# Kernel optimization log

Hardware: AMD Instinct MI355X
Metric: run time of the kernel (lower is better)

The kernel has to match this reference:

```python
import jax, jax.numpy as jnp
import numpy as np

EPS = 1e-9
N, E = 100000, 1000000
IN_F, OUT_F, HEADS = 128, 64, 2


def normalize_points(x):
    # UHG projective normalize: unit-norm spatial part, keep last (homogeneous) coord
    n = jnp.linalg.norm(x[..., :-1], axis=-1, keepdims=True)
    return jnp.concatenate([x[..., :-1] / jnp.maximum(n, EPS), x[..., -1:]], axis=-1)


def uhg_inner(a, b):
    # hyperbolic inner product: spatial dot minus time-time product
    return jnp.sum(a[..., :-1] * b[..., :-1], axis=-1) - a[..., -1] * b[..., -1]


def compute_cross_ratio(p1, p2, p3, p4):
    num = uhg_inner(p1, p3) * uhg_inner(p2, p4)
    den = uhg_inner(p1, p4) * uhg_inner(p2, p3)
    return num / jnp.where(jnp.abs(den) < EPS, EPS, den)


def restore_cross_ratio(x, cr_target):
    cr_cur = compute_cross_ratio(x[0], x[1], x[2], x[3])
    scale = jnp.abs(cr_target / jnp.where(jnp.abs(cr_cur) < EPS, EPS, cr_cur)) ** 0.25
    return x * scale


def setup_inputs() -> dict:
    key = jax.random.key(0)
    ks = jax.random.split(key, 10)
    s_in = 1.0 / np.sqrt(IN_F)
    s_hid = 1.0 / np.sqrt(OUT_F * HEADS)
    H = OUT_F * HEADS
    return {
        "x": jax.random.normal(ks[0], (N, IN_F), dtype=jnp.float32),
        "edge_index": jax.random.randint(ks[1], (2, E), 0, N, dtype=jnp.int64),
        "Wq": jax.random.uniform(ks[2], (H, IN_F), jnp.float32, -s_in, s_in),
        "bq": jnp.zeros((H,), jnp.float32),
        "Wk": jax.random.uniform(ks[3], (H, IN_F), jnp.float32, -s_in, s_in),
        "bk": jnp.zeros((H,), jnp.float32),
        "Wv": jax.random.uniform(ks[4], (H, IN_F), jnp.float32, -s_in, s_in),
        "bv": jnp.zeros((H,), jnp.float32),
        "Wo": jax.random.uniform(ks[5], (OUT_F, H), jnp.float32, -s_hid, s_hid),
        "bo": jnp.zeros((OUT_F,), jnp.float32),
    }


def reference(x, edge_index, Wq, bq, Wk, bk, Wv, bv, Wo, bo):
    n = x.shape[0]
    cr_initial = compute_cross_ratio(x[0], x[1], x[2], x[3])
    x_proj = normalize_points(x)
    q = (x_proj @ Wq.T + bq).reshape(n, HEADS, OUT_F)
    k = (x_proj @ Wk.T + bk).reshape(n, HEADS, OUT_F)
    v = (x_proj @ Wv.T + bv).reshape(n, HEADS, OUT_F)
    row, col = edge_index[0], edge_index[1]
    qe = normalize_points(q[row])  # [E, H, D]
    ke = normalize_points(k[col])
    scores = uhg_inner(qe, ke) / np.sqrt(IN_F)  # [E, H]
    alpha = jax.nn.softmax(scores, axis=0)  # global softmax over edges (as in source)
    msgs = v[col] * alpha[..., None]  # [E, H, D]
    out = jax.ops.segment_sum(msgs, row, num_segments=n)  # [N, H, D]
    out = out.reshape(n, HEADS * OUT_F)
    out = out @ Wo.T + bo
    out = restore_cross_ratio(out, cr_initial)
    return out
```

## Files before the change

### kernel.cpp

```cpp
#include <hip/hip_runtime.h>
#include <math.h>

#define EPSF 1e-9f
#define INV_SQRT128 0.08838834764831845f

typedef _Float16 half8 __attribute__((ext_vector_type(8)));
typedef float f32x4 __attribute__((ext_vector_type(4)));

__device__ __forceinline__ void gl_lds16(const void* g, void* l) {
    __builtin_amdgcn_global_load_lds((const __attribute__((address_space(1))) void*)g,
                                     (__attribute__((address_space(3))) void*)l, 16, 0, 0);
}

__global__ void k_wpack(const float* __restrict__ Wq, const float* __restrict__ Wk,
                        const float* __restrict__ Wv, half8* __restrict__ whi,
                        half8* __restrict__ wlo, float* __restrict__ w127) {
    int t = blockIdx.x * 256 + threadIdx.x;
    if (t >= 6144) return;
    int col = t & 127, g = (t >> 7) & 3, ks = (t >> 9) & 3, kind = t >> 11;
    const float* W = (kind == 0) ? Wq : (kind == 1) ? Wk : Wv;
    const float4* W4 = (const float4*)W;
    float4 a = W4[col * 32 + ks * 8 + g * 2];
    float4 b = W4[col * 32 + ks * 8 + g * 2 + 1];
    float xv[8] = {a.x, a.y, a.z, a.w, b.x, b.y, b.z, b.w};
    half8 h, lo;
#pragma unroll
    for (int j = 0; j < 8; j++) {
        _Float16 hh = (_Float16)xv[j];
        h[j] = hh;
        lo[j] = (_Float16)((xv[j] - (float)hh) * 4096.0f);
    }
    whi[t] = h;
    wlo[t] = lo;
    if (ks == 3 && g == 3) w127[kind * 128 + col] = xv[7];
}

__global__ void k_wpack2(const float* __restrict__ Wo, half8* __restrict__ wohi,
                         half8* __restrict__ wolo) {
    int t = blockIdx.x * 256 + threadIdx.x;
    if (t >= 1024) return;
    int col = t & 63, g = (t >> 6) & 3, ks = t >> 8;
    const float4* W4 = (const float4*)Wo;
    float4 a = W4[col * 32 + ks * 8 + g * 2];
    float4 b = W4[col * 32 + ks * 8 + g * 2 + 1];
    float xv[8] = {a.x, a.y, a.z, a.w, b.x, b.y, b.z, b.w};
    half8 h, lo;
#pragma unroll
    for (int j = 0; j < 8; j++) {
        _Float16 hh = (_Float16)xv[j];
        h[j] = hh;
        lo[j] = (_Float16)((xv[j] - (float)hh) * 4096.0f);
    }
    wohi[t] = h;
    wolo[t] = lo;
}

__global__ void __launch_bounds__(256, 2)
k_qkvm(const float* __restrict__ x,
       const half8* __restrict__ whi, const half8* __restrict__ wlo,
       const float* __restrict__ w127,
       const float* __restrict__ bq, const float* __restrict__ bk,
       const float* __restrict__ bv,
       float* __restrict__ qn, float* __restrict__ kvout,
       const int* __restrict__ ei, int* __restrict__ bcnt,
       int N, int E, int chunk) {
    int b = (int)blockIdx.x;
    __shared__ half8 bsh[4096];
    if (b < 512 && (b & 1)) {
        int* h = (int*)bsh;
        int t = threadIdx.x;
        int hid = b >> 1;
        h[t] = 0;
        __syncthreads();
        int s = hid * chunk, e1 = min(s + chunk, E);
        for (int e = s + t; e < e1; e += 256) atomicAdd(&h[ei[e] >> 9], 1);
        __syncthreads();
        bcnt[hid * 256 + t] = h[t];
        return;
    }
    int gb = (b < 512) ? (b >> 1) : (b - 256);

    int tid = threadIdx.x;
    int wv = tid >> 6;
    int l = tid & 63;
    int r = l & 15;
    int g = l >> 4;
    int rowbase = gb * 128 + wv * 32;
    const float4* x4 = (const float4*)x;

    {
        const half8* sH = whi + wv * 512;
        const half8* sL = wlo + wv * 512;
#pragma unroll
        for (int i = 0; i < 8; i++) {
            gl_lds16(sH + i * 64 + l, bsh + wv * 512 + i * 64);
            gl_lds16(sL + i * 64 + l, bsh + 2048 + wv * 512 + i * 64);
        }
    }

    half8 hiA[2][4], loA[2][4];
    float rnj[2][4], tcj[2][4];
#pragma unroll
    for (int t = 0; t < 2; t++) {
        int row = min(rowbase + t * 16 + r, N - 1);
        float ssum = 0.f, tl = 0.f;
#pragma unroll
        for (int ks = 0; ks < 4; ks++) {
            float4 a = x4[(size_t)row * 32 + ks * 8 + g * 2];
            float4 bb = x4[(size_t)row * 32 + ks * 8 + g * 2 + 1];
            float xv[8] = {a.x, a.y, a.z, a.w, bb.x, bb.y, bb.z, bb.w};
#pragma unroll
            for (int j = 0; j < 8; j++) {
                _Float16 hh = (_Float16)xv[j];
                hiA[t][ks][j] = hh;
                loA[t][ks][j] = (_Float16)((xv[j] - (float)hh) * 4096.0f);
                ssum += xv[j] * xv[j];
            }
            if (ks == 3 && g == 3) { tl = xv[7]; ssum -= xv[7] * xv[7]; }
        }
        ssum += __shfl_xor(ssum, 16);
        ssum += __shfl_xor(ssum, 32);
        float rn = 1.f / fmaxf(sqrtf(ssum), EPSF);
        float tla = __shfl(tl, 48 + r);
        float tc = tla * (1.f - rn);
#pragma unroll
        for (int j = 0; j < 4; j++) {
            rnj[t][j] = __shfl(rn, g * 4 + j);
            tcj[t][j] = __shfl(tc, g * 4 + j);
        }
    }

    asm volatile("s_waitcnt vmcnt(0)" ::: "memory");
    __syncthreads();

    const float* const bks[3] = {bq, bk, bv};
    bool lane15 = (r == 15);
    const f32x4 zz = {0.f, 0.f, 0.f, 0.f};
    int dsbase = g * 128 + r;

    for (int kind = 0; kind < 3; kind++) {
        float wcA[2][4], bbA[2][4];
#pragma unroll
        for (int h = 0; h < 2; h++)
#pragma unroll
            for (int ct = 0; ct < 4; ct++) {
                int col = (h * 4 + ct) * 16 + r;
                wcA[h][ct] = w127[kind * 128 + col];
                bbA[h][ct] = bks[kind][col];
            }

#pragma unroll
        for (int h = 0; h < 2; h++) {
            f32x4 aM[2][4], aX[2][4];
#pragma unroll
            for (int t = 0; t < 2; t++)
#pragma unroll
                for (int ct = 0; ct < 4; ct++) { aM[t][ct] = zz; aX[t][ct] = zz; }

#pragma unroll
            for (int ks = 0; ks < 4; ks++) {
                half8 hB[4], lB[4];
#pragma unroll
                for (int ct = 0; ct < 4; ct++) {
                    int bi = dsbase + ks * 512 + (h * 4 + ct) * 16;
                    hB[ct] = bsh[bi];
                    lB[ct] = bsh[2048 + bi];
                }
#pragma unroll
                for (int ct = 0; ct < 4; ct++) {
                    aM[0][ct] = __builtin_amdgcn_mfma_f32_16x16x32_f16(hiA[0][ks], hB[ct], aM[0][ct], 0, 0, 0);
                    aM[1][ct] = __builtin_amdgcn_mfma_f32_16x16x32_f16(hiA[1][ks], hB[ct], aM[1][ct], 0, 0, 0);
                    aX[0][ct] = __builtin_amdgcn_mfma_f32_16x16x32_f16(hiA[0][ks], lB[ct], aX[0][ct], 0, 0, 0);
                    aX[0][ct] = __builtin_amdgcn_mfma_f32_16x16x32_f16(loA[0][ks], hB[ct], aX[0][ct], 0, 0, 0);
                    aX[1][ct] = __builtin_amdgcn_mfma_f32_16x16x32_f16(hiA[1][ks], lB[ct], aX[1][ct], 0, 0, 0);
                    aX[1][ct] = __builtin_amdgcn_mfma_f32_16x16x32_f16(loA[1][ks], hB[ct], aX[1][ct], 0, 0, 0);
                }
            }

#pragma unroll
            for (int t = 0; t < 2; t++) {
                float cv[4][4];
#pragma unroll
                for (int ct = 0; ct < 4; ct++)
#pragma unroll
                    for (int j = 0; j < 4; j++) {
                        float acc = aM[t][ct][j] + aX[t][ct][j] * (1.0f / 4096.0f);
                        cv[ct][j] = fmaf(rnj[t][j], acc, fmaf(tcj[t][j], wcA[h][ct], bbA[h][ct]));
                    }
                if (kind < 2) {
#pragma unroll
                    for (int j = 0; j < 4; j++) {
                        float ss = 0.f;
#pragma unroll
                        for (int ct = 0; ct < 4; ct++) {
                            float c = cv[ct][j];
                            ss += (ct == 3 && lane15) ? 0.f : c * c;
                        }
                        ss += __shfl_xor(ss, 1);
                        ss += __shfl_xor(ss, 2);
                        ss += __shfl_xor(ss, 4);
                        ss += __shfl_xor(ss, 8);
                        float rh = 1.f / fmaxf(sqrtf(ss), EPSF);
#pragma unroll
                        for (int ct = 0; ct < 4; ct++) {
                            bool ist = (ct == 3) && lane15;
                            if (!ist) cv[ct][j] *= rh;
                            if (kind == 0) {
                                if (ist) cv[ct][j] = -cv[ct][j];
                                cv[ct][j] *= INV_SQRT128;
                            }
                        }
                    }
                }
#pragma unroll
                for (int j = 0; j < 4; j++) {
                    int row = rowbase + t * 16 + g * 4 + j;
                    if (row < N) {
                        float* dst = (kind == 0)
                            ? (qn + (size_t)row * 128)
                            : (kvout + (size_t)row * 256 + (kind == 2 ? 128 : 0));
#pragma unroll
                        for (int ct = 0; ct < 4; ct++)
                            dst[(h * 4 + ct) * 16 + r] = cv[ct][j];
                    }
                }
            }
        }

        if (kind < 2) {
            __syncthreads();
            const half8* sH = whi + (kind + 1) * 2048 + wv * 512;
            const half8* sL = wlo + (kind + 1) * 2048 + wv * 512;
#pragma unroll
            for (int i = 0; i < 8; i++) {
                gl_lds16(sH + i * 64 + l, bsh + wv * 512 + i * 64);
                gl_lds16(sL + i * 64 + l, bsh + 2048 + wv * 512 + i * 64);
            }
            asm volatile("s_waitcnt vmcnt(0)" ::: "memory");
            __syncthreads();
        }
    }
}

__global__ void k_bin2(int* __restrict__ bcnt, int* __restrict__ bintot) {
    __shared__ int sd[256];
    int b = blockIdx.x, t = threadIdx.x;
    int v = bcnt[t * 256 + b];
    sd[t] = v;
    __syncthreads();
    for (int off = 1; off < 256; off <<= 1) {
        int val = sd[t];
        int add = (t >= off) ? sd[t - off] : 0;
        __syncthreads();
        sd[t] = val + add;
        __syncthreads();
    }
    bcnt[t * 256 + b] = sd[t] - v;
    if (t == 255) bintot[b] = sd[255];
}

__global__ void k_bin3(const int* __restrict__ bintot, int* __restrict__ binoff,
                       int* __restrict__ offs, int N, int E) {
    __shared__ int sd[256];
    int t = threadIdx.x;
    int v = bintot[t];
    sd[t] = v;
    __syncthreads();
    for (int off = 1; off < 256; off <<= 1) {
        int val = sd[t];
        int add = (t >= off) ? sd[t - off] : 0;
        __syncthreads();
        sd[t] = val + add;
        __syncthreads();
    }
    binoff[t] = sd[t] - v;
    if (t == 255) {
        binoff[256] = sd[255];
        offs[N] = E;
    }
}

__global__ void k_scat1(const int* __restrict__ ei, const int* __restrict__ bcnt,
                        const int* __restrict__ binoff, int* __restrict__ packed,
                        int E, int chunk) {
    __shared__ int cur[256];
    int t = threadIdx.x, b = blockIdx.x;
    cur[t] = binoff[t] + bcnt[b * 256 + t];
    __syncthreads();
    int s = b * chunk, e1 = min(s + chunk, E);
    for (int e = s + t; e < e1; e += 256) {
        int r = ei[e];
        int c = ei[E + e];
        int p = atomicAdd(&cur[r >> 9], 1);
        packed[p] = ((r & 511) << 17) | c;
    }
}

__global__ void __launch_bounds__(256)
k_sortf(const int* __restrict__ packed, const int* __restrict__ binoff,
        int* __restrict__ ccol, int* __restrict__ offs, int N) {
    __shared__ int seg[6656];
    __shared__ int h[512];
    __shared__ int sc[256];
    int b = blockIdx.x, t = threadIdx.x;
    int s = binoff[b], e1 = binoff[b + 1];
    int cnt = min(e1 - s, 6656);
    for (int i = t; i < cnt; i += 256) seg[i] = packed[s + i];
    h[t] = 0;
    h[t + 256] = 0;
    __syncthreads();
    for (int i = t; i < cnt; i += 256) atomicAdd(&h[seg[i] >> 17], 1);
    __syncthreads();
    int v0 = h[2 * t], v1 = h[2 * t + 1];
    int pair = v0 + v1;
    sc[t] = pair;
    __syncthreads();
    for (int off = 1; off < 256; off <<= 1) {
        int val = sc[t];
        int add = (t >= off) ? sc[t - off] : 0;
        __syncthreads();
        sc[t] = val + add;
        __syncthreads();
    }
    int pexcl = sc[t] - pair;
    __syncthreads();
    h[2 * t] = pexcl;
    h[2 * t + 1] = pexcl + v0;
    int rowbase = b << 9;
    if (rowbase + 2 * t < N) offs[rowbase + 2 * t] = s + h[2 * t];
    if (rowbase + 2 * t + 1 < N) offs[rowbase + 2 * t + 1] = s + h[2 * t + 1];
    __syncthreads();
    for (int i = t; i < cnt; i += 256) {
        int pk = seg[i];
        int p = atomicAdd(&h[pk >> 17], 1);
        ccol[s + p] = pk & 0x1FFFF;
    }
}

__global__ void k_edge(const float* __restrict__ qn, const float* __restrict__ kv,
                       const int* __restrict__ offs, const int* __restrict__ ccol,
                       float* __restrict__ U, double* __restrict__ psum, int N) {
    int g = threadIdx.x >> 5;
    int l = threadIdx.x & 31;
    int head = l >> 4;
    int n = blockIdx.x * 8 + g;
    double esum = 0.0;
    if (n < N) {
        float4 q4 = ((const float4*)qn)[(size_t)n * 32 + l];
        int s0 = offs[n], s1 = offs[n + 1];
        float4 acc = {0.f, 0.f, 0.f, 0.f};
        const float4* kv4 = (const float4*)kv;
        int i = s0;
        for (; i + 4 <= s1; i += 4) {
            int c0 = ccol[i];
            int c1 = ccol[i + 1];
            int c2 = ccol[i + 2];
            int c3 = ccol[i + 3];
            float4 ka = kv4[(size_t)c0 * 64 + l];
            float4 va = kv4[(size_t)c0 * 64 + 32 + l];
            float4 kb = kv4[(size_t)c1 * 64 + l];
            float4 vb = kv4[(size_t)c1 * 64 + 32 + l];
            float4 kc = kv4[(size_t)c2 * 64 + l];
            float4 vc = kv4[(size_t)c2 * 64 + 32 + l];
            float4 kd = kv4[(size_t)c3 * 64 + l];
            float4 vd = kv4[(size_t)c3 * 64 + 32 + l];
            float p0 = q4.x * ka.x;
            p0 = fmaf(q4.y, ka.y, p0); p0 = fmaf(q4.z, ka.z, p0); p0 = fmaf(q4.w, ka.w, p0);
            float p1 = q4.x * kb.x;
            p1 = fmaf(q4.y, kb.y, p1); p1 = fmaf(q4.z, kb.z, p1); p1 = fmaf(q4.w, kb.w, p1);
            float p2 = q4.x * kc.x;
            p2 = fmaf(q4.y, kc.y, p2); p2 = fmaf(q4.z, kc.z, p2); p2 = fmaf(q4.w, kc.w, p2);
            float p3 = q4.x * kd.x;
            p3 = fmaf(q4.y, kd.y, p3); p3 = fmaf(q4.z, kd.z, p3); p3 = fmaf(q4.w, kd.w, p3);
            p0 += __shfl_xor(p0, 1); p1 += __shfl_xor(p1, 1);
            p2 += __shfl_xor(p2, 1); p3 += __shfl_xor(p3, 1);
            p0 += __shfl_xor(p0, 2); p1 += __shfl_xor(p1, 2);
            p2 += __shfl_xor(p2, 2); p3 += __shfl_xor(p3, 2);
            p0 += __shfl_xor(p0, 4); p1 += __shfl_xor(p1, 4);
            p2 += __shfl_xor(p2, 4); p3 += __shfl_xor(p3, 4);
            p0 += __shfl_xor(p0, 8); p1 += __shfl_xor(p1, 8);
            p2 += __shfl_xor(p2, 8); p3 += __shfl_xor(p3, 8);
            float e0 = expf(p0);
            float e1 = expf(p1);
            float e2 = expf(p2);
            float e3 = expf(p3);
            acc.x = fmaf(va.x, e0, acc.x); acc.y = fmaf(va.y, e0, acc.y);
            acc.z = fmaf(va.z, e0, acc.z); acc.w = fmaf(va.w, e0, acc.w);
            acc.x = fmaf(vb.x, e1, acc.x); acc.y = fmaf(vb.y, e1, acc.y);
            acc.z = fmaf(vb.z, e1, acc.z); acc.w = fmaf(vb.w, e1, acc.w);
            acc.x = fmaf(vc.x, e2, acc.x); acc.y = fmaf(vc.y, e2, acc.y);
            acc.z = fmaf(vc.z, e2, acc.z); acc.w = fmaf(vc.w, e2, acc.w);
            acc.x = fmaf(vd.x, e3, acc.x); acc.y = fmaf(vd.y, e3, acc.y);
            acc.z = fmaf(vd.z, e3, acc.z); acc.w = fmaf(vd.w, e3, acc.w);
            esum += (double)((e0 + e1) + (e2 + e3));
        }
        for (; i < s1; i++) {
            int c = ccol[i];
            float4 k4 = kv4[(size_t)c * 64 + l];
            float4 v4 = kv4[(size_t)c * 64 + 32 + l];
            float p = q4.x * k4.x;
            p = fmaf(q4.y, k4.y, p); p = fmaf(q4.z, k4.z, p); p = fmaf(q4.w, k4.w, p);
            p += __shfl_xor(p, 1);
            p += __shfl_xor(p, 2);
            p += __shfl_xor(p, 4);
            p += __shfl_xor(p, 8);
            float e = expf(p);
            acc.x = fmaf(v4.x, e, acc.x); acc.y = fmaf(v4.y, e, acc.y);
            acc.z = fmaf(v4.z, e, acc.z); acc.w = fmaf(v4.w, e, acc.w);
            esum += (double)e;
        }
        ((float4*)U)[(size_t)n * 32 + l] = acc;
    }
    __shared__ double sd[2][8];
    if ((l & 15) == 0) sd[head][g] = esum;
    __syncthreads();
    if (threadIdx.x < 2) {
        double s = 0.0;
        for (int i2 = 0; i2 < 8; i2++) s += sd[threadIdx.x][i2];
        psum[(size_t)blockIdx.x * 2 + threadIdx.x] = s;
    }
}

__global__ void k_crout4(const float* __restrict__ x, const float* __restrict__ U,
                         const float* __restrict__ Wo, const float* __restrict__ bo,
                         const double* __restrict__ psum, int P,
                         double* __restrict__ sumf, float* __restrict__ scalef) {
    __shared__ float xs[4 * 128];
    __shared__ float o4[4 * 64];
    __shared__ double crin_sh;
    __shared__ double sdr[2][4];
    int tid = threadIdx.x;
    {
        double s0 = 0.0, s1 = 0.0;
        for (int i = tid; i < P; i += 256) {
            s0 += psum[2 * i];
            s1 += psum[2 * i + 1];
        }
        for (int off = 32; off; off >>= 1) {
            s0 += __shfl_xor(s0, off);
            s1 += __shfl_xor(s1, off);
        }
        int w = tid >> 6;
        if ((tid & 63) == 0) { sdr[0][w] = s0; sdr[1][w] = s1; }
    }
    xs[tid] = U[tid];
    xs[tid + 256] = U[tid + 256];
    __syncthreads();
    if (tid == 0) {
        double s0 = sdr[0][0] + sdr[0][1] + sdr[0][2] + sdr[0][3];
        double s1 = sdr[1][0] + sdr[1][1] + sdr[1][2] + sdr[1][3];
        sumf[0] = s0;
        sumf[1] = s1;
    }
    if (tid >= 64 && tid < 128) {
        int l = tid - 64;
        const int pa[4] = {0, 1, 0, 1};
        const int pb[4] = {2, 3, 3, 2};
        double inner[4];
        for (int p = 0; p < 4; p++) {
            const float* a = x + pa[p] * 128;
            const float* b = x + pb[p] * 128;
            double s = (double)a[l] * (double)b[l];
            double t = (double)a[l + 64] * (double)b[l + 64];
            s += (l == 63) ? -t : t;
            for (int off = 32; off; off >>= 1) s += __shfl_xor(s, off);
            inner[p] = s;
        }
        if (l == 0) {
            double num = inner[0] * inner[1];
            double den = inner[2] * inner[3];
            if (fabs(den) < 1e-9) den = 1e-9;
            crin_sh = num / den;
        }
    }
    __syncthreads();
    int w = tid >> 6, o = tid & 63;
    float si0 = (float)(1.0 / sumf[0]);
    float si1 = (float)(1.0 / sumf[1]);
    const float* xr = xs + w * 128;
    const float* wr = Wo + (size_t)o * 128;
    float d0 = 0.f, d1 = 0.f;
    for (int j = 0; j < 64; j++) d0 = fmaf(xr[j], wr[j], d0);
    for (int j = 64; j < 128; j++) d1 = fmaf(xr[j], wr[j], d1);
    o4[w * 64 + o] = d0 * si0 + d1 * si1 + bo[o];
    __syncthreads();
    if (tid < 64) {
        int l = tid;
        const int pa[4] = {0, 1, 0, 1};
        const int pb[4] = {2, 3, 3, 2};
        double inner[4];
        for (int p = 0; p < 4; p++) {
            double t = (double)o4[pa[p] * 64 + l] * (double)o4[pb[p] * 64 + l];
            if (l == 63) t = -t;
            for (int off = 32; off; off >>= 1) t += __shfl_xor(t, off);
            inner[p] = t;
        }
        if (l == 0) {
            double num = inner[0] * inner[1];
            double den = inner[2] * inner[3];
            if (fabs(den) < 1e-9) den = 1e-9;
            double crc = num / den;
            if (fabs(crc) < 1e-9) crc = 1e-9;
            double ratio = crin_sh / crc;
            scalef[0] = (float)pow(fabs(ratio), 0.25);
        }
    }
}

__global__ void __launch_bounds__(256, 2)
k_outm(const float* __restrict__ U, const half8* __restrict__ wohi,
       const half8* __restrict__ wolo, const float* __restrict__ bo,
       const double* __restrict__ sumf, const float* __restrict__ scalef,
       float* __restrict__ out, int N) {
    __shared__ half8 bsh[2048];
    int tid = threadIdx.x;
    int wv = tid >> 6;
    int l = tid & 63;
    int r = l & 15;
    int g = l >> 4;
    int rowbase = blockIdx.x * 128 + wv * 32;

    {
        const half8* sH = wohi + wv * 256;
        const half8* sL = wolo + wv * 256;
#pragma unroll
        for (int i = 0; i < 4; i++) {
            gl_lds16(sH + i * 64 + l, bsh + wv * 256 + i * 64);
            gl_lds16(sL + i * 64 + l, bsh + 1024 + wv * 256 + i * 64);
        }
    }

    float si0 = (float)(1.0 / sumf[0]);
    float si1 = (float)(1.0 / sumf[1]);
    const float4* U4 = (const float4*)U;
    half8 hiA[2][4], loA[2][4];
#pragma unroll
    for (int t = 0; t < 2; t++) {
        int row = min(rowbase + t * 16 + r, N - 1);
#pragma unroll
        for (int ks = 0; ks < 4; ks++) {
            float si = (ks < 2) ? si0 : si1;
            float4 a = U4[(size_t)row * 32 + ks * 8 + g * 2];
            float4 b = U4[(size_t)row * 32 + ks * 8 + g * 2 + 1];
            float xv[8] = {a.x, a.y, a.z, a.w, b.x, b.y, b.z, b.w};
#pragma unroll
            for (int j = 0; j < 8; j++) {
                float v = xv[j] * si;
                _Float16 hh = (_Float16)v;
                hiA[t][ks][j] = hh;
                loA[t][ks][j] = (_Float16)((v - (float)hh) * 4096.0f);
            }
        }
    }

    asm volatile("s_waitcnt vmcnt(0)" ::: "memory");
    __syncthreads();

    const f32x4 zz = {0.f, 0.f, 0.f, 0.f};
    f32x4 aM[2][4], aX[2][4];
#pragma unroll
    for (int t = 0; t < 2; t++)
#pragma unroll
        for (int ct = 0; ct < 4; ct++) { aM[t][ct] = zz; aX[t][ct] = zz; }

#pragma unroll
    for (int ks = 0; ks < 4; ks++) {
        half8 hB[4], lB[4];
#pragma unroll
        for (int ct = 0; ct < 4; ct++) {
            int bi = ks * 256 + g * 64 + ct * 16 + r;
            hB[ct] = bsh[bi];
            lB[ct] = bsh[1024 + bi];
        }
#pragma unroll
        for (int ct = 0; ct < 4; ct++) {
            aM[0][ct] = __builtin_amdgcn_mfma_f32_16x16x32_f16(hiA[0][ks], hB[ct], aM[0][ct], 0, 0, 0);
            aM[1][ct] = __builtin_amdgcn_mfma_f32_16x16x32_f16(hiA[1][ks], hB[ct], aM[1][ct], 0, 0, 0);
            aX[0][ct] = __builtin_amdgcn_mfma_f32_16x16x32_f16(hiA[0][ks], lB[ct], aX[0][ct], 0, 0, 0);
            aX[0][ct] = __builtin_amdgcn_mfma_f32_16x16x32_f16(loA[0][ks], hB[ct], aX[0][ct], 0, 0, 0);
            aX[1][ct] = __builtin_amdgcn_mfma_f32_16x16x32_f16(hiA[1][ks], lB[ct], aX[1][ct], 0, 0, 0);
            aX[1][ct] = __builtin_amdgcn_mfma_f32_16x16x32_f16(loA[1][ks], hB[ct], aX[1][ct], 0, 0, 0);
        }
    }

    float sf = scalef[0];
#pragma unroll
    for (int t = 0; t < 2; t++)
#pragma unroll
        for (int ct = 0; ct < 4; ct++) {
            float bb = bo[ct * 16 + r];
#pragma unroll
            for (int j = 0; j < 4; j++) {
                int row = rowbase + t * 16 + g * 4 + j;
                if (row < N) {
                    float c = (aM[t][ct][j] + aX[t][ct][j] * (1.0f / 4096.0f) + bb) * sf;
                    out[(size_t)row * 64 + ct * 16 + r] = c;
                }
            }
        }
}

extern "C" void kernel_launch(void* const* d_in, const int* in_sizes, int n_in,
                              void* d_out, int out_size, void* d_ws, size_t ws_size,
                              hipStream_t stream) {
    const float* x  = (const float*)d_in[0];
    const int*   ei = (const int*)d_in[1];
    const float* Wq = (const float*)d_in[2];
    const float* bq = (const float*)d_in[3];
    const float* Wk = (const float*)d_in[4];
    const float* bk = (const float*)d_in[5];
    const float* Wv = (const float*)d_in[6];
    const float* bv = (const float*)d_in[7];
    const float* Wo = (const float*)d_in[8];
    const float* bo = (const float*)d_in[9];
    float* out = (float*)d_out;

    const int N = in_sizes[0] / 128;
    const int E = in_sizes[1] / 2;
    const size_t NR = (size_t)N * 128;
    const int NGB = (N + 127) / 128;
    const int GB = (N + 7) / 8;
    const int chunk = (E + 255) / 256;
    const int NBINS = (N + 511) >> 9;

    float* qn = (float*)d_ws;
    float* kv = qn + NR;
    int* offs = (int*)(kv + NR * 2);
    int* ccol = offs + N + 2;
    int* bcnt = ccol + E;
    int* bintot = bcnt + 256 * 256;
    int* binoff = bintot + 256;
    uintptr_t pd = ((uintptr_t)(binoff + 257 + 1) + 7) & ~(uintptr_t)7;
    double* psum = (double*)pd;
    double* sumf = psum + (size_t)GB * 2;
    float* scalef = (float*)(sumf + 2);

    uintptr_t pw = ((uintptr_t)ccol + 15) & ~(uintptr_t)15;
    half8* whi = (half8*)pw;
    half8* wlo = whi + 6144;
    float* w127 = (float*)(wlo + 6144);

    uintptr_t pw2 = ((uintptr_t)bcnt + 15) & ~(uintptr_t)15;
    half8* wohi = (half8*)pw2;
    half8* wolo = wohi + 1024;

    float* U = qn;

    k_wpack<<<24, 256, 0, stream>>>(Wq, Wk, Wv, whi, wlo, w127);
    k_qkvm<<<NGB + 256, 256, 0, stream>>>(x, whi, wlo, w127, bq, bk, bv,
                                          qn, kv, ei, bcnt, N, E, chunk);
    k_bin2<<<256, 256, 0, stream>>>(bcnt, bintot);
    k_bin3<<<1, 256, 0, stream>>>(bintot, binoff, offs, N, E);
    k_scat1<<<256, 256, 0, stream>>>(ei, bcnt, binoff, ccol, E, chunk);
    k_wpack2<<<4, 256, 0, stream>>>(Wo, wohi, wolo);
    k_sortf<<<NBINS, 256, 0, stream>>>(ccol, binoff, ccol, offs, N);
    k_edge<<<GB, 256, 0, stream>>>(qn, kv, offs, ccol, U, psum, N);
    k_crout4<<<1, 256, 0, stream>>>(x, U, Wo, bo, psum, GB, sumf, scalef);
    k_outm<<<NGB, 256, 0, stream>>>(U, wohi, wolo, bo, sumf, scalef, out, N);
}
```

Baseline: 423.4 us.

## Split edge kernel into score and aggregation passes with separate K/V arrays

Splits the fused edge kernel into k_score, which gathers K, computes exp scores and stores them per edge and head, and k_aggr, which gathers V and accumulates weighted sums. K and V move from an interleaved layout to separate arrays, so each pass gathers a 51 MB working set instead of 102 MB. The aim is a better L2/LLC hit rate on the random gathers. The cost is an extra kernel launch, an 8 MB score write and read, and a second pass over the CSR indices.

Result: faster. 406.7 us (-3.9%).

```diff
diff --git a/kernel.cpp b/kernel.cpp
--- a/kernel.cpp
+++ b/kernel.cpp
@@ -61,7 +61,7 @@
        const float* __restrict__ w127,
        const float* __restrict__ bq, const float* __restrict__ bk,
        const float* __restrict__ bv,
-       float* __restrict__ qn, float* __restrict__ kvout,
+       float* __restrict__ qn, float* __restrict__ kn, float* __restrict__ vn,
        const int* __restrict__ ei, int* __restrict__ bcnt,
        int N, int E, int chunk) {
     int b = (int)blockIdx.x;
@@ -216,9 +216,8 @@
                 for (int j = 0; j < 4; j++) {
                     int row = rowbase + t * 16 + g * 4 + j;
                     if (row < N) {
-                        float* dst = (kind == 0)
-                            ? (qn + (size_t)row * 128)
-                            : (kvout + (size_t)row * 256 + (kind == 2 ? 128 : 0));
+                        float* dst = (kind == 0) ? qn : (kind == 1 ? kn : vn);
+                        dst += (size_t)row * 128;
 #pragma unroll
                         for (int ct = 0; ct < 4; ct++)
                             dst[(h * 4 + ct) * 16 + r] = cv[ct][j];
@@ -337,9 +336,9 @@
     }
 }
 
-__global__ void k_edge(const float* __restrict__ qn, const float* __restrict__ kv,
-                       const int* __restrict__ offs, const int* __restrict__ ccol,
-                       float* __restrict__ U, double* __restrict__ psum, int N) {
+__global__ void k_score(const float* __restrict__ qn, const float* __restrict__ kn,
+                        const int* __restrict__ offs, const int* __restrict__ ccol,
+                        float* __restrict__ e2, double* __restrict__ psum, int N, int E) {
     int g = threadIdx.x >> 5;
     int l = threadIdx.x & 31;
     int head = l >> 4;
@@ -348,22 +347,18 @@
     if (n < N) {
         float4 q4 = ((const float4*)qn)[(size_t)n * 32 + l];
         int s0 = offs[n], s1 = offs[n + 1];
-        float4 acc = {0.f, 0.f, 0.f, 0.f};
-        const float4* kv4 = (const float4*)kv;
+        const float4* k4p = (const float4*)kn;
+        float* eh = e2 + (size_t)head * E;
         int i = s0;
         for (; i + 4 <= s1; i += 4) {
             int c0 = ccol[i];
             int c1 = ccol[i + 1];
             int c2 = ccol[i + 2];
             int c3 = ccol[i + 3];
-            float4 ka = kv4[(size_t)c0 * 64 + l];
-            float4 va = kv4[(size_t)c0 * 64 + 32 + l];
-            float4 kb = kv4[(size_t)c1 * 64 + l];
-            float4 vb = kv4[(size_t)c1 * 64 + 32 + l];
-            float4 kc = kv4[(size_t)c2 * 64 + l];
-            float4 vc = kv4[(size_t)c2 * 64 + 32 + l];
-            float4 kd = kv4[(size_t)c3 * 64 + l];
-            float4 vd = kv4[(size_t)c3 * 64 + 32 + l];
+            float4 ka = k4p[(size_t)c0 * 32 + l];
+            float4 kb = k4p[(size_t)c1 * 32 + l];
+            float4 kc = k4p[(size_t)c2 * 32 + l];
+            float4 kd = k4p[(size_t)c3 * 32 + l];
             float p0 = q4.x * ka.x;
             p0 = fmaf(q4.y, ka.y, p0); p0 = fmaf(q4.z, ka.z, p0); p0 = fmaf(q4.w, ka.w, p0);
             float p1 = q4.x * kb.x;
@@ -380,36 +375,33 @@
             p2 += __shfl_xor(p2, 4); p3 += __shfl_xor(p3, 4);
             p0 += __shfl_xor(p0, 8); p1 += __shfl_xor(p1, 8);
             p2 += __shfl_xor(p2, 8); p3 += __shfl_xor(p3, 8);
-            float e0 = expf(p0);
-            float e1 = expf(p1);
-            float e2 = expf(p2);
-            float e3 = expf(p3);
-            acc.x = fmaf(va.x, e0, acc.x); acc.y = fmaf(va.y, e0, acc.y);
-            acc.z = fmaf(va.z, e0, acc.z); acc.w = fmaf(va.w, e0, acc.w);
-            acc.x = fmaf(vb.x, e1, acc.x); acc.y = fmaf(vb.y, e1, acc.y);
-            acc.z = fmaf(vb.z, e1, acc.z); acc.w = fmaf(vb.w, e1, acc.w);
-            acc.x = fmaf(vc.x, e2, acc.x); acc.y = fmaf(vc.y, e2, acc.y);
-            acc.z = fmaf(vc.z, e2, acc.z); acc.w = fmaf(vc.w, e2, acc.w);
-            acc.x = fmaf(vd.x, e3, acc.x); acc.y = fmaf(vd.y, e3, acc.y);
-            acc.z = fmaf(vd.z, e3, acc.z); acc.w = fmaf(vd.w, e3, acc.w);
-            esum += (double)((e0 + e1) + (e2 + e3));
+            float x0 = expf(p0);
+            float x1 = expf(p1);
+            float x2 = expf(p2);
+            float x3 = expf(p3);
+            if ((l & 15) == 0) {
+                eh[i] = x0;
+                eh[i + 1] = x1;
+                eh[i + 2] = x2;
+                eh[i + 3] = x3;
+                esum += (double)((x0 + x1) + (x2 + x3));
+            }
         }
         for (; i < s1; i++) {
             int c = ccol[i];
-            float4 k4 = kv4[(size_t)c * 64 + l];
-            float4 v4 = kv4[(size_t)c * 64 + 32 + l];
+            float4 k4 = k4p[(size_t)c * 32 + l];
             float p = q4.x * k4.x;
             p = fmaf(q4.y, k4.y, p); p = fmaf(q4.z, k4.z, p); p = fmaf(q4.w, k4.w, p);
             p += __shfl_xor(p, 1);
             p += __shfl_xor(p, 2);
             p += __shfl_xor(p, 4);
             p += __shfl_xor(p, 8);
-            float e = expf(p);
-            acc.x = fmaf(v4.x, e, acc.x); acc.y = fmaf(v4.y, e, acc.y);
-            acc.z = fmaf(v4.z, e, acc.z); acc.w = fmaf(v4.w, e, acc.w);
-            esum += (double)e;
-        }
-        ((float4*)U)[(size_t)n * 32 + l] = acc;
+            float x = expf(p);
+            if ((l & 15) == 0) {
+                eh[i] = x;
+                esum += (double)x;
+            }
+        }
     }
     __shared__ double sd[2][8];
     if ((l & 15) == 0) sd[head][g] = esum;
@@ -419,6 +411,51 @@
         for (int i2 = 0; i2 < 8; i2++) s += sd[threadIdx.x][i2];
         psum[(size_t)blockIdx.x * 2 + threadIdx.x] = s;
     }
+}
+
+__global__ void k_aggr(const float* __restrict__ vn, const int* __restrict__ offs,
+                       const int* __restrict__ ccol, const float* __restrict__ e2,
+                       float* __restrict__ U, int N, int E) {
+    int g = threadIdx.x >> 5;
+    int l = threadIdx.x & 31;
+    int head = l >> 4;
+    int n = blockIdx.x * 8 + g;
+    if (n >= N) return;
+    int s0 = offs[n], s1 = offs[n + 1];
+    const float4* v4p = (const float4*)vn;
+    const float* eh = e2 + (size_t)head * E;
+    float4 acc = {0.f, 0.f, 0.f, 0.f};
+    int i = s0;
+    for (; i + 4 <= s1; i += 4) {
+        int c0 = ccol[i];
+        int c1 = ccol[i + 1];
+        int c2 = ccol[i + 2];
+        int c3 = ccol[i + 3];
+        float4 va = v4p[(size_t)c0 * 32 + l];
+        float4 vb = v4p[(size_t)c1 * 32 + l];
+        float4 vc = v4p[(size_t)c2 * 32 + l];
+        float4 vd = v4p[(size_t)c3 * 32 + l];
+        float x0 = eh[i];
+        float x1 = eh[i + 1];
+        float x2 = eh[i + 2];
+        float x3 = eh[i + 3];
+        acc.x = fmaf(va.x, x0, acc.x); acc.y = fmaf(va.y, x0, acc.y);
+        acc.z = fmaf(va.z, x0, acc.z); acc.w = fmaf(va.w, x0, acc.w);
+        acc.x = fmaf(vb.x, x1, acc.x); acc.y = fmaf(vb.y, x1, acc.y);
+        acc.z = fmaf(vb.z, x1, acc.z); acc.w = fmaf(vb.w, x1, acc.w);
+        acc.x = fmaf(vc.x, x2, acc.x); acc.y = fmaf(vc.y, x2, acc.y);
+        acc.z = fmaf(vc.z, x2, acc.z); acc.w = fmaf(vc.w, x2, acc.w);
+        acc.x = fmaf(vd.x, x3, acc.x); acc.y = fmaf(vd.y, x3, acc.y);
+        acc.z = fmaf(vd.z, x3, acc.z); acc.w = fmaf(vd.w, x3, acc.w);
+    }
+    for (; i < s1; i++) {
+        int c = ccol[i];
+        float4 v4 = v4p[(size_t)c * 32 + l];
+        float x = eh[i];
+        acc.x = fmaf(v4.x, x, acc.x); acc.y = fmaf(v4.y, x, acc.y);
+        acc.z = fmaf(v4.z, x, acc.z); acc.w = fmaf(v4.w, x, acc.w);
+    }
+    ((float4*)U)[(size_t)n * 32 + l] = acc;
 }
 
 __global__ void k_crout4(const float* __restrict__ x, const float* __restrict__ U,
@@ -624,13 +661,16 @@
     const int NBINS = (N + 511) >> 9;
 
     float* qn = (float*)d_ws;
-    float* kv = qn + NR;
-    int* offs = (int*)(kv + NR * 2);
+    float* kn = qn + NR;
+    float* vn = kn + NR;
+    int* offs = (int*)(vn + NR);
     int* ccol = offs + N + 2;
     int* bcnt = ccol + E;
     int* bintot = bcnt + 256 * 256;
     int* binoff = bintot + 256;
-    uintptr_t pd = ((uintptr_t)(binoff + 257 + 1) + 7) & ~(uintptr_t)7;
+    uintptr_t pe = ((uintptr_t)(binoff + 257 + 1) + 15) & ~(uintptr_t)15;
+    float* e2 = (float*)pe;
+    uintptr_t pd = ((uintptr_t)(e2 + 2 * (size_t)E) + 7) & ~(uintptr_t)7;
     double* psum = (double*)pd;
     double* sumf = psum + (size_t)GB * 2;
     float* scalef = (float*)(sumf + 2);
@@ -648,13 +688,14 @@
 
     k_wpack<<<24, 256, 0, stream>>>(Wq, Wk, Wv, whi, wlo, w127);
     k_qkvm<<<NGB + 256, 256, 0, stream>>>(x, whi, wlo, w127, bq, bk, bv,
-                                          qn, kv, ei, bcnt, N, E, chunk);
+                                          qn, kn, vn, ei, bcnt, N, E, chunk);
     k_bin2<<<256, 256, 0, stream>>>(bcnt, bintot);
     k_bin3<<<1, 256, 0, stream>>>(bintot, binoff, offs, N, E);
     k_scat1<<<256, 256, 0, stream>>>(ei, bcnt, binoff, ccol, E, chunk);
     k_wpack2<<<4, 256, 0, stream>>>(Wo, wohi, wolo);
     k_sortf<<<NBINS, 256, 0, stream>>>(ccol, binoff, ccol, offs, N);
-    k_edge<<<GB, 256, 0, stream>>>(qn, kv, offs, ccol, U, psum, N);
+    k_score<<<GB, 256, 0, stream>>>(qn, kn, offs, ccol, e2, psum, N, E);
+    k_aggr<<<GB, 256, 0, stream>>>(vn, offs, ccol, e2, U, N, E);
     k_crout4<<<1, 256, 0, stream>>>(x, U, Wo, bo, psum, GB, sumf, scalef);
     k_outm<<<NGB, 256, 0, stream>>>(U, wohi, wolo, bo, sumf, scalef, out, N);
 }
```
